# Performance work log

Measured on AMD Instinct MI355X. Metric: run time of the kernel, lower is better.

## Reference

```python
import jax, jax.numpy as jnp
import numpy as np

B, S, D, H = 4, 2048, 256, 8
DH = D // H
DFF = 4 * D
EPS = 1e-5


def _layernorm(x, w, b):
    mu = jnp.mean(x, axis=-1, keepdims=True)
    var = jnp.mean((x - mu) ** 2, axis=-1, keepdims=True)
    return (x - mu) * jax.lax.rsqrt(var + EPS) * w + b


def setup_inputs() -> dict:
    key = jax.random.key(0)
    ks = jax.random.split(key, 16)
    s = 0.02
    return {
        "x": jax.random.normal(ks[0], (B, S, D), jnp.float32),
        "in_proj_w": jax.random.normal(ks[1], (3 * D, D), jnp.float32) * s,
        "in_proj_b": jax.random.normal(ks[2], (3 * D,), jnp.float32) * s,
        "out_w": jax.random.normal(ks[3], (D, D), jnp.float32) * s,
        "out_b": jax.random.normal(ks[4], (D,), jnp.float32) * s,
        "ln1_w": jnp.ones((D,), jnp.float32),
        "ln1_b": jnp.zeros((D,), jnp.float32),
        "ln2_w": jnp.ones((D,), jnp.float32),
        "ln2_b": jnp.zeros((D,), jnp.float32),
        "ff1_w": jax.random.normal(ks[5], (DFF, D), jnp.float32) * s,
        "ff1_b": jax.random.normal(ks[6], (DFF,), jnp.float32) * s,
        "ff2_w": jax.random.normal(ks[7], (D, DFF), jnp.float32) * s,
        "ff2_b": jax.random.normal(ks[8], (D,), jnp.float32) * s,
        "slopes": jax.random.normal(ks[9], (H, 1, 1), jnp.float32),
    }


def reference(x, in_proj_w, in_proj_b, out_w, out_b, ln1_w, ln1_b, ln2_w, ln2_b,
              ff1_w, ff1_b, ff2_w, ff2_b, slopes):
    # learned ALiBi-style relative bias: (H, S, S)
    pos = jnp.arange(S, dtype=jnp.float32)
    rel = jnp.abs(pos[None, :] - pos[:, None])          # (S, S)
    bias = -jnp.abs(slopes) * rel[None, :, :]           # (H, S, S)

    xn = _layernorm(x, ln1_w, ln1_b)
    qkv = jnp.einsum('bsd,ed->bse', xn, in_proj_w) + in_proj_b
    q, k, v = jnp.split(qkv, 3, axis=-1)
    # (B, H, S, DH)
    q = q.reshape(B, S, H, DH).transpose(0, 2, 1, 3)
    k = k.reshape(B, S, H, DH).transpose(0, 2, 1, 3)
    v = v.reshape(B, S, H, DH).transpose(0, 2, 1, 3)

    scores = jnp.einsum('bhqd,bhkd->bhqk', q, k) / jnp.sqrt(jnp.float32(DH))
    scores = scores + bias[None, :, :, :]
    attn = jax.nn.softmax(scores, axis=-1)
    ctx = jnp.einsum('bhqk,bhkd->bhqd', attn, v)
    ctx = ctx.transpose(0, 2, 1, 3).reshape(B, S, D)
    attn_out = jnp.einsum('bsd,ed->bse', ctx, out_w) + out_b

    x = x + attn_out
    xn2 = _layernorm(x, ln2_w, ln2_b)
    h = jnp.einsum('bsd,fd->bsf', xn2, ff1_w) + ff1_b
    h = jax.nn.gelu(h, approximate=False)
    ff_out = jnp.einsum('bsf,df->bsd', h, ff2_w) + ff2_b
    return x + ff_out
```

## Files before the change

### kernel.cpp

```cpp
#include <hip/hip_runtime.h>
#include <hip/hip_bf16.h>
#include <math.h>

#define S_LEN 2048
#define D_MODEL 256
#define N_HEADS 8
#define HEAD_DIM 32
#define D_FF 1024
#define ROWS_TOTAL 8192

typedef __attribute__((ext_vector_type(8))) short short8;
typedef __attribute__((ext_vector_type(4))) float f32x4;

__device__ inline ushort f2bf(float f) {
    unsigned u = __builtin_bit_cast(unsigned, f);
    unsigned r = (u + 0x7fffu + ((u >> 16) & 1u)) >> 16;
    return (ushort)r;
}

__device__ inline float bf2f(ushort u) {
    return __builtin_bit_cast(float, ((unsigned)u) << 16);
}

__device__ inline unsigned cvtpk(float a, float b) {
    unsigned r;
    asm("v_cvt_pk_bf16_f32 %0, %1, %2" : "=v"(r) : "v"(a), "v"(b));
    return r;
}

__global__ __launch_bounds__(256) void prep_kernel(
    const float* __restrict__ w0, const float* __restrict__ w1,
    const float* __restrict__ w2, const float* __restrict__ w3,
    ushort* __restrict__ o0, ushort* __restrict__ o1,
    ushort* __restrict__ o2, ushort* __restrict__ o3,
    const float* __restrict__ x, const float* __restrict__ lnw,
    const float* __restrict__ lnb, ushort* __restrict__ xnb) {
    int blk = blockIdx.x;
    if (blk < 768) {
        int i = blk * 256 + threadIdx.x;
        const float* src;
        ushort* dst;
        int off;
        if (i < 49152)       { src = w0; dst = o0; off = i; }
        else if (i < 65536)  { src = w1; dst = o1; off = i - 49152; }
        else if (i < 131072) { src = w2; dst = o2; off = i - 65536; }
        else                 { src = w3; dst = o3; off = i - 131072; }
        float4 v = ((const float4*)src)[off];
        ushort4 u = {f2bf(v.x), f2bf(v.y), f2bf(v.z), f2bf(v.w)};
        ((ushort4*)dst)[off] = u;
    } else {
        int wid = threadIdx.x >> 6, lane = threadIdx.x & 63;
        int row = (blk - 768) * 4 + wid;
        float4 v = ((const float4*)(x + (size_t)row * D_MODEL))[lane];
        float4 wv = ((const float4*)lnw)[lane];
        float4 bv = ((const float4*)lnb)[lane];
        float s = v.x + v.y + v.z + v.w;
        float s2 = v.x * v.x + v.y * v.y + v.z * v.z + v.w * v.w;
        #pragma unroll
        for (int off = 1; off < 64; off <<= 1) {
            s  += __shfl_xor(s, off);
            s2 += __shfl_xor(s2, off);
        }
        float mu = s * (1.0f / D_MODEL);
        float var = s2 * (1.0f / D_MODEL) - mu * mu;
        float rstd = rsqrtf(var + 1e-5f);
        ushort4 o = {f2bf((v.x - mu) * rstd * wv.x + bv.x), f2bf((v.y - mu) * rstd * wv.y + bv.y),
                     f2bf((v.z - mu) * rstd * wv.z + bv.z), f2bf((v.w - mu) * rstd * wv.w + bv.w)};
        ((ushort4*)(xnb + (size_t)row * D_MODEL))[lane] = o;
    }
}

template <int EPI, int BM, int BN>
__global__ __launch_bounds__(256) void gemm_mfma(
    const ushort* __restrict__ A,
    const ushort* __restrict__ W,
    const float* __restrict__ bias,
    const void* __restrict__ resid,
    float* __restrict__ outf,
    ushort* __restrict__ outh,
    ushort* __restrict__ qout, ushort* __restrict__ kout, ushort* __restrict__ vout,
    int M, int N, int K) {
    constexpr int MR = BM / 32;
    constexpr int NR = BN / 32;
    __shared__ ushort As[BM * 64];
    __shared__ ushort Bs[BN * 64];
    const int tid = threadIdx.x;
    const int lane = tid & 63, wid = tid >> 6;
    const int l15 = lane & 15, hi = lane >> 4;
    const int wr = wid >> 1, wc = wid & 1;
    const int row0 = blockIdx.x * BM, col0 = blockIdx.y * BN;

    f32x4 acc[MR][NR];
    #pragma unroll
    for (int m = 0; m < MR; m++)
        #pragma unroll
        for (int n = 0; n < NR; n++) acc[m][n] = (f32x4){0.f, 0.f, 0.f, 0.f};

    short8 sa[MR], sb[NR];
    #pragma unroll
    for (int t = 0; t < MR; t++) {
        int c = tid + t * 256;
        sa[t] = *(const short8*)(A + (size_t)(row0 + (c >> 3)) * K + (c & 7) * 8);
    }
    #pragma unroll
    for (int t = 0; t < NR; t++) {
        int c = tid + t * 256;
        sb[t] = *(const short8*)(W + (size_t)(col0 + (c >> 3)) * K + (c & 7) * 8);
    }

    for (int k0 = 0; k0 < K; k0 += 64) {
        __syncthreads();
        #pragma unroll
        for (int t = 0; t < MR; t++) {
            int c = tid + t * 256;
            int r = c >> 3, cb = (c & 7) * 16;
            *(short8*)((char*)As + r * 128 + (cb ^ ((r & 7) << 4))) = sa[t];
        }
        #pragma unroll
        for (int t = 0; t < NR; t++) {
            int c = tid + t * 256;
            int r = c >> 3, cb = (c & 7) * 16;
            *(short8*)((char*)Bs + r * 128 + (cb ^ ((r & 7) << 4))) = sb[t];
        }
        __syncthreads();
        if (k0 + 64 < K) {
            #pragma unroll
            for (int t = 0; t < MR; t++) {
                int c = tid + t * 256;
                sa[t] = *(const short8*)(A + (size_t)(row0 + (c >> 3)) * K + k0 + 64 + (c & 7) * 8);
            }
            #pragma unroll
            for (int t = 0; t < NR; t++) {
                int c = tid + t * 256;
                sb[t] = *(const short8*)(W + (size_t)(col0 + (c >> 3)) * K + k0 + 64 + (c & 7) * 8);
            }
        }
        #pragma unroll
        for (int ks = 0; ks < 2; ks++) {
            short8 af[MR], bfr[NR];
            #pragma unroll
            for (int m = 0; m < MR; m++) {
                int r = wr * (BM / 2) + m * 16 + l15;
                af[m] = *(const short8*)((char*)As + r * 128 + ((ks * 64 + hi * 16) ^ ((r & 7) << 4)));
            }
            #pragma unroll
            for (int n = 0; n < NR; n++) {
                int r = wc * (BN / 2) + n * 16 + l15;
                bfr[n] = *(const short8*)((char*)Bs + r * 128 + ((ks * 64 + hi * 16) ^ ((r & 7) << 4)));
            }
            #pragma unroll
            for (int m = 0; m < MR; m++)
                #pragma unroll
                for (int n = 0; n < NR; n++)
                    acc[m][n] = __builtin_amdgcn_mfma_f32_16x16x32_bf16(af[m], bfr[n], acc[m][n], 0, 0, 0);
        }
    }

    #pragma unroll
    for (int m = 0; m < MR; m++) {
        #pragma unroll
        for (int n = 0; n < NR; n++) {
            #pragma unroll
            for (int r = 0; r < 4; r++) {
                int row = row0 + wr * (BM / 2) + m * 16 + hi * 4 + r;
                int col = col0 + wc * (BN / 2) + n * 16 + l15;
                float val = acc[m][n][r] + bias[col];
                if (EPI == 0) {
                    int part = col >> 8;
                    int d_o = col & 255;
                    int hh = d_o >> 5, dh = d_o & 31;
                    int bbb = row >> 11, s = row & 2047;
                    size_t bhi = (size_t)bbb * N_HEADS + hh;
                    if (part == 0) {
                        qout[(bhi * S_LEN + s) * HEAD_DIM + dh] = f2bf(val * 0.2550347137f);
                    } else {
                        int tt = s >> 6, k = s & 63;
                        size_t tb = (bhi * 32 + tt) * 2048;
                        if (part == 1)
                            kout[tb + (dh >> 3) * 512 + k * 8 + (dh & 7)] = f2bf(val);
                        else
                            vout[tb + ((size_t)((k >> 5) * 4 + ((k >> 3) & 3))) * 256 + dh * 8 + (k & 7)] = f2bf(val);
                    }
                } else if (EPI == 2) {
                    float g = 0.5f * val * (1.f + erff(val * 0.70710678118654752f));
                    outh[(size_t)row * N + col] = f2bf(g);
                } else {
                    float rv = bf2f(((const ushort*)resid)[(size_t)row * N + col]);
                    outf[(size_t)row * N + col] = rv + val;
                }
            }
        }
    }
}

__global__ __launch_bounds__(256) void gemm_opln(
    const ushort* __restrict__ A,
    const ushort* __restrict__ W,
    const float* __restrict__ bias,
    const float* __restrict__ residf,
    const float* __restrict__ lnw, const float* __restrict__ lnb,
    ushort* __restrict__ xnb, ushort* __restrict__ x1b) {
    __shared__ ushort As[16 * 64];
    __shared__ ushort Bs[256 * 64];
    __shared__ float red[4][16][2];
    const int tid = threadIdx.x;
    const int lane = tid & 63, wc = tid >> 6;
    const int l15 = lane & 15, hi = lane >> 4;
    const int row0 = blockIdx.x * 16;

    f32x4 acc[4];
    #pragma unroll
    for (int n = 0; n < 4; n++) acc[n] = (f32x4){0.f, 0.f, 0.f, 0.f};

    short8 sa, sb[8];
    if (tid < 128)
        sa = *(const short8*)(A + (size_t)(row0 + (tid >> 3)) * 256 + (tid & 7) * 8);
    #pragma unroll
    for (int t = 0; t < 8; t++) {
        int c = tid + t * 256;
        sb[t] = *(const short8*)(W + (size_t)(c >> 3) * 256 + (c & 7) * 8);
    }

    for (int k0 = 0; k0 < 256; k0 += 64) {
        __syncthreads();
        if (tid < 128) {
            int r = tid >> 3, cb = (tid & 7) * 16;
            *(short8*)((char*)As + r * 128 + (cb ^ ((r & 7) << 4))) = sa;
        }
        #pragma unroll
        for (int t = 0; t < 8; t++) {
            int c = tid + t * 256;
            int r = c >> 3, cb = (c & 7) * 16;
            *(short8*)((char*)Bs + r * 128 + (cb ^ ((r & 7) << 4))) = sb[t];
        }
        __syncthreads();
        if (k0 + 64 < 256) {
            if (tid < 128)
                sa = *(const short8*)(A + (size_t)(row0 + (tid >> 3)) * 256 + k0 + 64 + (tid & 7) * 8);
            #pragma unroll
            for (int t = 0; t < 8; t++) {
                int c = tid + t * 256;
                sb[t] = *(const short8*)(W + (size_t)(c >> 3) * 256 + k0 + 64 + (c & 7) * 8);
            }
        }
        #pragma unroll
        for (int ks = 0; ks < 2; ks++) {
            short8 af, bfr[4];
            {
                int r = l15;
                af = *(const short8*)((char*)As + r * 128 + ((ks * 64 + hi * 16) ^ ((r & 7) << 4)));
            }
            #pragma unroll
            for (int n = 0; n < 4; n++) {
                int r = wc * 64 + n * 16 + l15;
                bfr[n] = *(const short8*)((char*)Bs + r * 128 + ((ks * 64 + hi * 16) ^ ((r & 7) << 4)));
            }
            #pragma unroll
            for (int n = 0; n < 4; n++)
                acc[n] = __builtin_amdgcn_mfma_f32_16x16x32_bf16(af, bfr[n], acc[n], 0, 0, 0);
        }
    }

    float x1v[4][4];
    float s1[4], s2[4];
    #pragma unroll
    for (int r = 0; r < 4; r++) { s1[r] = 0.f; s2[r] = 0.f; }
    #pragma unroll
    for (int n = 0; n < 4; n++) {
        #pragma unroll
        for (int r = 0; r < 4; r++) {
            int row = row0 + hi * 4 + r;
            int col = wc * 64 + n * 16 + l15;
            float v = acc[n][r] + bias[col] + residf[(size_t)row * 256 + col];
            x1v[n][r] = v;
            s1[r] += v;
            s2[r] += v * v;
        }
    }
    #pragma unroll
    for (int r = 0; r < 4; r++) {
        #pragma unroll
        for (int off = 1; off < 16; off <<= 1) {
            s1[r] += __shfl_xor(s1[r], off);
            s2[r] += __shfl_xor(s2[r], off);
        }
    }
    if (l15 == 0) {
        #pragma unroll
        for (int r = 0; r < 4; r++) {
            red[wc][hi * 4 + r][0] = s1[r];
            red[wc][hi * 4 + r][1] = s2[r];
        }
    }
    __syncthreads();
    #pragma unroll
    for (int r = 0; r < 4; r++) {
        int rl = hi * 4 + r;
        float a1 = red[0][rl][0] + red[1][rl][0] + red[2][rl][0] + red[3][rl][0];
        float a2 = red[0][rl][1] + red[1][rl][1] + red[2][rl][1] + red[3][rl][1];
        float mu = a1 * (1.0f / 256.f);
        float var = a2 * (1.0f / 256.f) - mu * mu;
        float rstd = rsqrtf(var + 1e-5f);
        size_t row = row0 + rl;
        #pragma unroll
        for (int n = 0; n < 4; n++) {
            int col = wc * 64 + n * 16 + l15;
            float v = x1v[n][r];
            xnb[row * 256 + col] = f2bf((v - mu) * rstd * lnw[col] + lnb[col]);
            x1b[row * 256 + col] = f2bf(v);
        }
    }
}

__global__ __launch_bounds__(256) void attn_mfma(
    const ushort* __restrict__ qb, const ushort* __restrict__ kb,
    const ushort* __restrict__ vt, const float* __restrict__ slopes,
    ushort* __restrict__ ctxout) {
    __shared__ ushort plds[4][1024];
    const int tid = threadIdx.x;
    const int wid = tid >> 6, lane = tid & 63;
    const int l15 = lane & 15, hi = lane >> 4;
    const int bh = blockIdx.y, h = bh & (N_HEADS - 1), bb = bh >> 3;
    const int qt = blockIdx.x * 4 + wid;
    const int qbase = qt * 16;
    const float slope = fabsf(slopes[h]) * 1.4426950408889634f;

    const int wl = (int)fminf(2048.f, 32.f / fmaxf(slope, 1e-6f));
    const int tlo = max(0, (qbase - wl) >> 6);
    const int thi = min(31, (qbase + 15 + wl) >> 6);

    const ushort* Kg = kb + (size_t)bh * 32 * 2048;
    const ushort* Vg = vt + (size_t)bh * 32 * 2048;

    short8 qf = *(const short8*)(qb + ((size_t)bh * S_LEN + qbase + l15) * HEAD_DIM + hi * 8);

    f32x4 ctxa[2];
    ctxa[0] = (f32x4){0.f, 0.f, 0.f, 0.f};
    ctxa[1] = (f32x4){0.f, 0.f, 0.f, 0.f};
    float lsum = 0.f;

    char* pw = (char*)&plds[wid][0];
    const int bpi = lane & 0x30;
    const int wr_off = ((hi >> 1) << 8) + (l15 << 4) + ((hi & 1) << 3);
    const int rd0 = (hi << 8) + (l15 << 4);

    const float qoff = (float)(qbase + l15 - 4 * hi);

    short8 kfc[4], vfc[2][2];
    {
        const ushort* Kt = Kg + (size_t)tlo * 2048;
        const ushort* Vt = Vg + (size_t)tlo * 2048;
        #pragma unroll
        for (int c = 0; c < 4; c++)
            kfc[c] = *(const short8*)(Kt + (hi * 64 + 16 * c + l15) * 8);
        #pragma unroll
        for (int f = 0; f < 2; f++)
            #pragma unroll
            for (int dt = 0; dt < 2; dt++)
                vfc[f][dt] = *(const short8*)(Vt + ((f * 4 + hi) * 32 + dt * 16 + l15) * 8);
    }

    for (int t = tlo; t <= thi; ++t) {
// ... 46 lines not shown
        short8 pa1 = *(const short8*)(pw + 1024 + rd0);
        __builtin_amdgcn_s_setprio(1);
        #pragma unroll
        for (int dt = 0; dt < 2; dt++) {
            ctxa[dt] = __builtin_amdgcn_mfma_f32_16x16x32_bf16(pa0, vfc[0][dt], ctxa[dt], 0, 0, 0);
            ctxa[dt] = __builtin_amdgcn_mfma_f32_16x16x32_bf16(pa1, vfc[1][dt], ctxa[dt], 0, 0, 0);
        }
        __builtin_amdgcn_s_setprio(0);

        #pragma unroll
        for (int c = 0; c < 4; c++) kfc[c] = kfn[c];
        #pragma unroll
        for (int f = 0; f < 2; f++)
            #pragma unroll
            for (int dt = 0; dt < 2; dt++) vfc[f][dt] = vfn[f][dt];
    }
    float inv = 1.f / lsum;
    int invi = __builtin_bit_cast(int, inv);
    #pragma unroll
    for (int r = 0; r < 4; r++) {
        float ir = __builtin_bit_cast(float, __builtin_amdgcn_ds_bpermute(bpi + 4 * r, invi));
        size_t row = (size_t)bb * S_LEN + qbase + 4 * hi + r;
        #pragma unroll
        for (int dt = 0; dt < 2; dt++)
            ctxout[row * D_MODEL + h * HEAD_DIM + dt * 16 + l15] = f2bf(ctxa[dt][r] * ir);
    }
}

extern "C" void kernel_launch(void* const* d_in, const int* in_sizes, int n_in,
                              void* d_out, int out_size, void* d_ws, size_t ws_size,
                              hipStream_t stream) {
    const float* x      = (const float*)d_in[0];
    const float* in_w   = (const float*)d_in[1];
    const float* in_b   = (const float*)d_in[2];
    const float* outw   = (const float*)d_in[3];
    const float* outb   = (const float*)d_in[4];
    const float* ln1w   = (const float*)d_in[5];
    const float* ln1b   = (const float*)d_in[6];
    const float* ln2w   = (const float*)d_in[7];
    const float* ln2b   = (const float*)d_in[8];
    const float* ff1w   = (const float*)d_in[9];
    const float* ff1b   = (const float*)d_in[10];
    const float* ff2w   = (const float*)d_in[11];
    const float* ff2b   = (const float*)d_in[12];
    const float* slopes = (const float*)d_in[13];
    float* out = (float*)d_out;

    const size_t SZ = (size_t)ROWS_TOTAL * D_MODEL;
    ushort* xnb   = (ushort*)d_ws;
    ushort* ctxb  = xnb + SZ;
    ushort* qb16  = ctxb + SZ;
    ushort* kb16  = qb16 + SZ;
    ushort* vt16  = kb16 + SZ;
    ushort* hbb   = vt16 + SZ;
    ushort* wqkvb = hbb + 4 * SZ;
    ushort* woutb = wqkvb + 768 * 256;
    ushort* wff1b = woutb + 256 * 256;
    ushort* wff2b = wff1b + 1024 * 256;
    ushort* x1b   = wff2b + 256 * 1024;

    prep_kernel<<<768 + ROWS_TOTAL / 4, 256, 0, stream>>>(
        in_w, outw, ff1w, ff2w, wqkvb, woutb, wff1b, wff2b, x, ln1w, ln1b, xnb);
    gemm_mfma<0, 64, 128><<<dim3(ROWS_TOTAL / 64, 768 / 128), 256, 0, stream>>>(
        xnb, wqkvb, in_b, nullptr, nullptr, nullptr, qb16, kb16, vt16, ROWS_TOTAL, 768, D_MODEL);
    attn_mfma<<<dim3(32, 32), 256, 0, stream>>>(qb16, kb16, vt16, slopes, ctxb);
    gemm_opln<<<ROWS_TOTAL / 16, 256, 0, stream>>>(
        ctxb, woutb, outb, x, ln2w, ln2b, xnb, x1b);
    gemm_mfma<2, 64, 128><<<dim3(ROWS_TOTAL / 64, D_FF / 128), 256, 0, stream>>>(
        xnb, wff1b, ff1b, nullptr, nullptr, hbb, nullptr, nullptr, nullptr, ROWS_TOTAL, D_FF, D_MODEL);
    gemm_mfma<5, 64, 64><<<dim3(ROWS_TOTAL / 64, D_MODEL / 64), 256, 0, stream>>>(
        hbb, wff2b, ff2b, x1b, out, nullptr, nullptr, nullptr, nullptr, ROWS_TOTAL, D_MODEL, D_FF);
}
```

Baseline: 74.85 us.

## Fuse FFN into one kernel and prepack weights into MFMA fragment layout

```diff
diff --git a/kernel.cpp b/kernel.cpp
--- a/kernel.cpp
+++ b/kernel.cpp
@@ -26,6 +26,16 @@
     unsigned r;
     asm("v_cvt_pk_bf16_f32 %0, %1, %2" : "=v"(r) : "v"(a), "v"(b));
     return r;
+}
+
+__device__ inline void cvt_frag(const float* __restrict__ src, ushort* __restrict__ dst,
+                                int off, int kshift, int NT) {
+    float4 v = ((const float4*)src)[off];
+    int n = off >> kshift;
+    int k = (off & ((1 << kshift) - 1)) << 2;
+    int idx = (((k >> 5) * NT + (n >> 4)) << 9) + (((k >> 3) & 3) << 7) + ((n & 15) << 3) + (k & 7);
+    ushort4 u = {f2bf(v.x), f2bf(v.y), f2bf(v.z), f2bf(v.w)};
+    *(ushort4*)(dst + idx) = u;
 }
 
 __global__ __launch_bounds__(256) void prep_kernel(
@@ -38,16 +48,10 @@
     int blk = blockIdx.x;
     if (blk < 768) {
         int i = blk * 256 + threadIdx.x;
-        const float* src;
-        ushort* dst;
-        int off;
-        if (i < 49152)       { src = w0; dst = o0; off = i; }
-        else if (i < 65536)  { src = w1; dst = o1; off = i - 49152; }
-        else if (i < 131072) { src = w2; dst = o2; off = i - 65536; }
-        else                 { src = w3; dst = o3; off = i - 131072; }
-        float4 v = ((const float4*)src)[off];
-        ushort4 u = {f2bf(v.x), f2bf(v.y), f2bf(v.z), f2bf(v.w)};
-        ((ushort4*)dst)[off] = u;
+        if (i < 49152)       cvt_frag(w0, o0, i, 6, 48);
+        else if (i < 65536)  cvt_frag(w1, o1, i - 49152, 6, 16);
+        else if (i < 131072) cvt_frag(w2, o2, i - 65536, 6, 64);
+        else                 cvt_frag(w3, o3, i - 131072, 8, 16);
     } else {
         int wid = threadIdx.x >> 6, lane = threadIdx.x & 63;
         int row = (blk - 768) * 4 + wid;
@@ -70,123 +74,75 @@
     }
 }
 
-template <int EPI, int BM, int BN>
-__global__ __launch_bounds__(256) void gemm_mfma(
+__global__ __launch_bounds__(256) void gemm_qkv(
     const ushort* __restrict__ A,
-    const ushort* __restrict__ W,
+    const ushort* __restrict__ Wt,
     const float* __restrict__ bias,
-    const void* __restrict__ resid,
-    float* __restrict__ outf,
-    ushort* __restrict__ outh,
-    ushort* __restrict__ qout, ushort* __restrict__ kout, ushort* __restrict__ vout,
-    int M, int N, int K) {
-    constexpr int MR = BM / 32;
-    constexpr int NR = BN / 32;
-    __shared__ ushort As[BM * 64];
-    __shared__ ushort Bs[BN * 64];
+    ushort* __restrict__ qout, ushort* __restrict__ kout, ushort* __restrict__ vout) {
+    __shared__ ushort As[64 * 256];
     const int tid = threadIdx.x;
     const int lane = tid & 63, wid = tid >> 6;
     const int l15 = lane & 15, hi = lane >> 4;
     const int wr = wid >> 1, wc = wid & 1;
-    const int row0 = blockIdx.x * BM, col0 = blockIdx.y * BN;
-
-    f32x4 acc[MR][NR];
-    #pragma unroll
-    for (int m = 0; m < MR; m++)
-        #pragma unroll
-        for (int n = 0; n < NR; n++) acc[m][n] = (f32x4){0.f, 0.f, 0.f, 0.f};
-
-    short8 sa[MR], sb[NR];
-    #pragma unroll
-    for (int t = 0; t < MR; t++) {
+    const int row0 = blockIdx.x * 64, col0 = blockIdx.y * 128;
+
+    #pragma unroll
+    for (int t = 0; t < 8; t++) {
         int c = tid + t * 256;
-        sa[t] = *(const short8*)(A + (size_t)(row0 + (c >> 3)) * K + (c & 7) * 8);
-    }
-    #pragma unroll
-    for (int t = 0; t < NR; t++) {
-        int c = tid + t * 256;
-        sb[t] = *(const short8*)(W + (size_t)(col0 + (c >> 3)) * K + (c & 7) * 8);
-    }
-
-    for (int k0 = 0; k0 < K; k0 += 64) {
-        __syncthreads();
-        #pragma unroll
-        for (int t = 0; t < MR; t++) {
-            int c = tid + t * 256;
-            int r = c >> 3, cb = (c & 7) * 16;
-            *(short8*)((char*)As + r * 128 + (cb ^ ((r & 7) << 4))) = sa[t];
-        }
-        #pragma unroll
-        for (int t = 0; t < NR; t++) {
-            int c = tid + t * 256;
-            int r = c >> 3, cb = (c & 7) * 16;
-            *(short8*)((char*)Bs + r * 128 + (cb ^ ((r & 7) << 4))) = sb[t];
-        }
-        __syncthreads();
-        if (k0 + 64 < K) {
-            #pragma unroll
-            for (int t = 0; t < MR; t++) {
-                int c = tid + t * 256;
-                sa[t] = *(const short8*)(A + (size_t)(row0 + (c >> 3)) * K + k0 + 64 + (c & 7) * 8);
-            }
-            #pragma unroll
-            for (int t = 0; t < NR; t++) {
-                int c = tid + t * 256;
-                sb[t] = *(const short8*)(W + (size_t)(col0 + (c >> 3)) * K + k0 + 64 + (c & 7) * 8);
-            }
-        }
-        #pragma unroll
-        for (int ks = 0; ks < 2; ks++) {
-            short8 af[MR], bfr[NR];
-            #pragma unroll
-            for (int m = 0; m < MR; m++) {
-                int r = wr * (BM / 2) + m * 16 + l15;
-                af[m] = *(const short8*)((char*)As + r * 128 + ((ks * 64 + hi * 16) ^ ((r & 7) << 4)));
-            }
-            #pragma unroll
-            for (int n = 0; n < NR; n++) {
-                int r = wc * (BN / 2) + n * 16 + l15;
-                bfr[n] = *(const short8*)((char*)Bs + r * 128 + ((ks * 64 + hi * 16) ^ ((r & 7) << 4)));
-            }
-            #pragma unroll
-            for (int m = 0; m < MR; m++)
-                #pragma unroll
-                for (int n = 0; n < NR; n++)
-                    acc[m][n] = __builtin_amdgcn_mfma_f32_16x16x32_bf16(af[m], bfr[n], acc[m][n], 0, 0, 0);
-        }
-    }
-
-    #pragma unroll
-    for (int m = 0; m < MR; m++) {
-        #pragma unroll
-        for (int n = 0; n < NR; n++) {
+        int r = c >> 5, cb = (c & 31) * 16;
+        short8 va = *(const short8*)(A + (size_t)(row0 + r) * 256 + (c & 31) * 8);
+        *(short8*)((char*)As + r * 512 + (cb ^ ((r & 7) << 4))) = va;
+    }
+    __syncthreads();
+
+    f32x4 acc[2][4];
+    #pragma unroll
+    for (int m = 0; m < 2; m++)
+        #pragma unroll
+        for (int n = 0; n < 4; n++) acc[m][n] = (f32x4){0.f, 0.f, 0.f, 0.f};
+
+    const int tn0 = (col0 >> 4) + wc * 4;
+    #pragma unroll
+    for (int tk = 0; tk < 8; tk++) {
+        short8 af[2], bfr[4];
+        #pragma unroll
+        for (int m = 0; m < 2; m++) {
+            int r = wr * 32 + m * 16 + l15;
+            af[m] = *(const short8*)((char*)As + r * 512 + ((tk * 64 + hi * 16) ^ ((r & 7) << 4)));
+        }
+        #pragma unroll
+        for (int n = 0; n < 4; n++)
+            bfr[n] = *(const short8*)(Wt + (((size_t)tk * 48 + tn0 + n) << 9) + lane * 8);
+        #pragma unroll
+        for (int m = 0; m < 2; m++)
+            #pragma unroll
+            for (int n = 0; n < 4; n++)
+                acc[m][n] = __builtin_amdgcn_mfma_f32_16x16x32_bf16(af[m], bfr[n], acc[m][n], 0, 0, 0);
+    }
+
+    #pragma unroll
+    for (int m = 0; m < 2; m++) {
+        #pragma unroll
+        for (int n = 0; n < 4; n++) {
             #pragma unroll
             for (int r = 0; r < 4; r++) {
-                int row = row0 + wr * (BM / 2) + m * 16 + hi * 4 + r;
-                int col = col0 + wc * (BN / 2) + n * 16 + l15;
+                int row = row0 + wr * 32 + m * 16 + hi * 4 + r;
+                int col = col0 + wc * 64 + n * 16 + l15;
                 float val = acc[m][n][r] + bias[col];
-                if (EPI == 0) {
-                    int part = col >> 8;
-                    int d_o = col & 255;
-                    int hh = d_o >> 5, dh = d_o & 31;
-                    int bbb = row >> 11, s = row & 2047;
-                    size_t bhi = (size_t)bbb * N_HEADS + hh;
-                    if (part == 0) {
-                        qout[(bhi * S_LEN + s) * HEAD_DIM + dh] = f2bf(val * 0.2550347137f);
-                    } else {
-                        int tt = s >> 6, k = s & 63;
-                        size_t tb = (bhi * 32 + tt) * 2048;
-                        if (part == 1)
-                            kout[tb + (dh >> 3) * 512 + k * 8 + (dh & 7)] = f2bf(val);
-                        else
-                            vout[tb + ((size_t)((k >> 5) * 4 + ((k >> 3) & 3))) * 256 + dh * 8 + (k & 7)] = f2bf(val);
-                    }
-                } else if (EPI == 2) {
-                    float g = 0.5f * val * (1.f + erff(val * 0.70710678118654752f));
-                    outh[(size_t)row * N + col] = f2bf(g);
+                int part = col >> 8;
+                int d_o = col & 255;
+                int hh = d_o >> 5, dh = d_o & 31;
+                int bbb = row >> 11, s = row & 2047;
+                size_t bhi = (size_t)bbb * N_HEADS + hh;
+                if (part == 0) {
+                    qout[(bhi * S_LEN + s) * HEAD_DIM + dh] = f2bf(val * 0.2550347137f);
                 } else {
-                    float rv = bf2f(((const ushort*)resid)[(size_t)row * N + col]);
-                    outf[(size_t)row * N + col] = rv + val;
+                    int tt = s >> 6, k = s & 63;
+                    size_t tb = (bhi * 32 + tt) * 2048;
+                    if (part == 1)
+                        kout[tb + (dh >> 3) * 512 + k * 8 + (dh & 7)] = f2bf(val);
+                    else
+                        vout[tb + ((size_t)((k >> 5) * 4 + ((k >> 3) & 3))) * 256 + dh * 8 + (k & 7)] = f2bf(val);
                 }
             }
         }
@@ -195,69 +151,38 @@
 
 __global__ __launch_bounds__(256) void gemm_opln(
     const ushort* __restrict__ A,
-    const ushort* __restrict__ W,
+    const ushort* __restrict__ Wt,
     const float* __restrict__ bias,
     const float* __restrict__ residf,
     const float* __restrict__ lnw, const float* __restrict__ lnb,
     ushort* __restrict__ xnb, ushort* __restrict__ x1b) {
-    __shared__ ushort As[16 * 64];
-    __shared__ ushort Bs[256 * 64];
+    __shared__ ushort As[16 * 256];
     __shared__ float red[4][16][2];
     const int tid = threadIdx.x;
-    const int lane = tid & 63, wc = tid >> 6;
+    const int lane = tid & 63, wid = tid >> 6;
     const int l15 = lane & 15, hi = lane >> 4;
     const int row0 = blockIdx.x * 16;
 
+    #pragma unroll
+    for (int t = 0; t < 2; t++) {
+        int c = tid + t * 256;
+        int r = c >> 5, cb = (c & 31) * 16;
+        short8 va = *(const short8*)(A + (size_t)(row0 + r) * 256 + (c & 31) * 8);
+        *(short8*)((char*)As + r * 512 + (cb ^ ((r & 7) << 4))) = va;
+    }
+    __syncthreads();
+
     f32x4 acc[4];
     #pragma unroll
     for (int n = 0; n < 4; n++) acc[n] = (f32x4){0.f, 0.f, 0.f, 0.f};
 
-    short8 sa, sb[8];
-    if (tid < 128)
-        sa = *(const short8*)(A + (size_t)(row0 + (tid >> 3)) * 256 + (tid & 7) * 8);
-    #pragma unroll
-    for (int t = 0; t < 8; t++) {
-        int c = tid + t * 256;
-        sb[t] = *(const short8*)(W + (size_t)(c >> 3) * 256 + (c & 7) * 8);
-    }
-
-    for (int k0 = 0; k0 < 256; k0 += 64) {
-        __syncthreads();
-        if (tid < 128) {
-            int r = tid >> 3, cb = (tid & 7) * 16;
-            *(short8*)((char*)As + r * 128 + (cb ^ ((r & 7) << 4))) = sa;
-        }
-        #pragma unroll
-        for (int t = 0; t < 8; t++) {
-            int c = tid + t * 256;
-            int r = c >> 3, cb = (c & 7) * 16;
-            *(short8*)((char*)Bs + r * 128 + (cb ^ ((r & 7) << 4))) = sb[t];
-        }
-        __syncthreads();
-        if (k0 + 64 < 256) {
-            if (tid < 128)
-                sa = *(const short8*)(A + (size_t)(row0 + (tid >> 3)) * 256 + k0 + 64 + (tid & 7) * 8);
-            #pragma unroll
-            for (int t = 0; t < 8; t++) {
-                int c = tid + t * 256;
-                sb[t] = *(const short8*)(W + (size_t)(c >> 3) * 256 + k0 + 64 + (c & 7) * 8);
-            }
-        }
-        #pragma unroll
-        for (int ks = 0; ks < 2; ks++) {
-            short8 af, bfr[4];
-            {
-                int r = l15;
-                af = *(const short8*)((char*)As + r * 128 + ((ks * 64 + hi * 16) ^ ((r & 7) << 4)));
-            }
-            #pragma unroll
-            for (int n = 0; n < 4; n++) {
-                int r = wc * 64 + n * 16 + l15;
-                bfr[n] = *(const short8*)((char*)Bs + r * 128 + ((ks * 64 + hi * 16) ^ ((r & 7) << 4)));
-            }
-            #pragma unroll
-            for (int n = 0; n < 4; n++)
-                acc[n] = __builtin_amdgcn_mfma_f32_16x16x32_bf16(af, bfr[n], acc[n], 0, 0, 0);
+    #pragma unroll
+    for (int tk = 0; tk < 8; tk++) {
+        short8 af = *(const short8*)((char*)As + l15 * 512 + ((tk * 64 + hi * 16) ^ ((l15 & 7) << 4)));
+        #pragma unroll
+        for (int n = 0; n < 4; n++) {
+            short8 bfr = *(const short8*)(Wt + (((size_t)tk * 16 + wid * 4 + n) << 9) + lane * 8);
+            acc[n] = __builtin_amdgcn_mfma_f32_16x16x32_bf16(af, bfr, acc[n], 0, 0, 0);
         }
     }
 
@@ -270,7 +195,7 @@
         #pragma unroll
         for (int r = 0; r < 4; r++) {
             int row = row0 + hi * 4 + r;
-            int col = wc * 64 + n * 16 + l15;
+            int col = wid * 64 + n * 16 + l15;
             float v = acc[n][r] + bias[col] + residf[(size_t)row * 256 + col];
             x1v[n][r] = v;
             s1[r] += v;
@@ -288,8 +213,8 @@
     if (l15 == 0) {
         #pragma unroll
         for (int r = 0; r < 4; r++) {
-            red[wc][hi * 4 + r][0] = s1[r];
-            red[wc][hi * 4 + r][1] = s2[r];
+            red[wid][hi * 4 + r][0] = s1[r];
+            red[wid][hi * 4 + r][1] = s2[r];
         }
     }
     __syncthreads();
@@ -304,10 +229,93 @@
         size_t row = row0 + rl;
         #pragma unroll
         for (int n = 0; n < 4; n++) {
-            int col = wc * 64 + n * 16 + l15;
+            int col = wid * 64 + n * 16 + l15;
             float v = x1v[n][r];
             xnb[row * 256 + col] = f2bf((v - mu) * rstd * lnw[col] + lnb[col]);
             x1b[row * 256 + col] = f2bf(v);
+        }
+    }
+}
+
+__global__ __launch_bounds__(256) void ffn_kernel(
+    const ushort* __restrict__ A,
+    const ushort* __restrict__ W1t,
+    const ushort* __restrict__ W2t,
+    const float* __restrict__ b1, const float* __restrict__ b2,
+    const ushort* __restrict__ x1b,
+    float* __restrict__ out) {
+    __shared__ ushort As[16 * 256];
+    __shared__ ushort Hs[2048];
+    const int tid = threadIdx.x;
+    const int lane = tid & 63, wid = tid >> 6;
+    const int l15 = lane & 15, hi = lane >> 4;
+    const int row0 = blockIdx.x * 16;
+
+    #pragma unroll
+    for (int t = 0; t < 2; t++) {
+        int c = tid + t * 256;
+        int r = c >> 5, cb = (c & 31) * 16;
+        short8 va = *(const short8*)(A + (size_t)(row0 + r) * 256 + (c & 31) * 8);
+        *(short8*)((char*)As + r * 512 + (cb ^ ((r & 7) << 4))) = va;
+    }
+    __syncthreads();
+
+    f32x4 acc[4];
+    #pragma unroll
+    for (int n = 0; n < 4; n++) acc[n] = (f32x4){0.f, 0.f, 0.f, 0.f};
+
+    const int hwr = (4 * wid + (hi >> 1)) * 256 + l15 * 16 + (hi & 1) * 8;
+
+    for (int ch = 0; ch < 8; ch++) {
+        f32x4 hacc[2];
+        hacc[0] = (f32x4){0.f, 0.f, 0.f, 0.f};
+        hacc[1] = (f32x4){0.f, 0.f, 0.f, 0.f};
+        #pragma unroll
+        for (int tk = 0; tk < 8; tk++) {
+            short8 xb = *(const short8*)((char*)As + l15 * 512 + ((tk * 64 + hi * 16) ^ ((l15 & 7) << 4)));
+            #pragma unroll
+            for (int nf = 0; nf < 2; nf++) {
+                int tnf = ch * 8 + wid * 2 + nf;
+                short8 fa = *(const short8*)(W1t + (((size_t)tk * 64 + tnf) << 9) + lane * 8);
+                hacc[nf] = __builtin_amdgcn_mfma_f32_16x16x32_bf16(fa, xb, hacc[nf], 0, 0, 0);
+            }
+        }
+        __syncthreads();
+        #pragma unroll
+        for (int nf = 0; nf < 2; nf++) {
+            int fcb = ch * 128 + wid * 32 + nf * 16 + hi * 4;
+            float g[4];
+            #pragma unroll
+            for (int r = 0; r < 4; r++) {
+                float v = hacc[nf][r] + b1[fcb + r];
+                g[r] = 0.5f * v * (1.f + erff(v * 0.70710678118654752f));
+            }
+            unsigned lo  = cvtpk(g[0], g[1]);
+            unsigned hi2 = cvtpk(g[2], g[3]);
+            *(unsigned long long*)((char*)Hs + (nf << 9) + hwr) =
+                ((unsigned long long)hi2 << 32) | (unsigned long long)lo;
+        }
+        __syncthreads();
+        #pragma unroll
+        for (int s = 0; s < 4; s++) {
+            short8 pa = *(const short8*)((char*)Hs + (4 * s + hi) * 256 + l15 * 16);
+            int tk2 = ch * 4 + s;
+            #pragma unroll
+            for (int n = 0; n < 4; n++) {
+                short8 bfr = *(const short8*)(W2t + (((size_t)tk2 * 16 + wid * 4 + n) << 9) + lane * 8);
+                acc[n] = __builtin_amdgcn_mfma_f32_16x16x32_bf16(pa, bfr, acc[n], 0, 0, 0);
+            }
+        }
+    }
+
+    #pragma unroll
+    for (int n = 0; n < 4; n++) {
+        #pragma unroll
+        for (int r = 0; r < 4; r++) {
+            size_t row = row0 + hi * 4 + r;
+            int col = wid * 64 + n * 16 + l15;
+            float rv = bf2f(x1b[row * 256 + col]);
+            out[row * 256 + col] = acc[n][r] + b2[col] + rv;
         }
     }
 }
@@ -460,22 +468,19 @@
     ushort* qb16  = ctxb + SZ;
     ushort* kb16  = qb16 + SZ;
     ushort* vt16  = kb16 + SZ;
-    ushort* hbb   = vt16 + SZ;
-    ushort* wqkvb = hbb + 4 * SZ;
-    ushort* woutb = wqkvb + 768 * 256;
-    ushort* wff1b = woutb + 256 * 256;
-    ushort* wff2b = wff1b + 1024 * 256;
-    ushort* x1b   = wff2b + 256 * 1024;
+    ushort* x1b   = vt16 + SZ;
+    ushort* wqkvt = x1b + SZ;
+    ushort* woutt = wqkvt + 768 * 256;
+    ushort* wff1t = woutt + 256 * 256;
+    ushort* wff2t = wff1t + 1024 * 256;
 
     prep_kernel<<<768 + ROWS_TOTAL / 4, 256, 0, stream>>>(
-        in_w, outw, ff1w, ff2w, wqkvb, woutb, wff1b, wff2b, x, ln1w, ln1b, xnb);
-    gemm_mfma<0, 64, 128><<<dim3(ROWS_TOTAL / 64, 768 / 128), 256, 0, stream>>>(
-        xnb, wqkvb, in_b, nullptr, nullptr, nullptr, qb16, kb16, vt16, ROWS_TOTAL, 768, D_MODEL);
+        in_w, outw, ff1w, ff2w, wqkvt, woutt, wff1t, wff2t, x, ln1w, ln1b, xnb);
+    gemm_qkv<<<dim3(ROWS_TOTAL / 64, 6), 256, 0, stream>>>(
+        xnb, wqkvt, in_b, qb16, kb16, vt16);
     attn_mfma<<<dim3(32, 32), 256, 0, stream>>>(qb16, kb16, vt16, slopes, ctxb);
     gemm_opln<<<ROWS_TOTAL / 16, 256, 0, stream>>>(
-        ctxb, woutb, outb, x, ln2w, ln2b, xnb, x1b);
-    gemm_mfma<2, 64, 128><<<dim3(ROWS_TOTAL / 64, D_FF / 128), 256, 0, stream>>>(
-        xnb, wff1b, ff1b, nullptr, nullptr, hbb, nullptr, nullptr, nullptr, ROWS_TOTAL, D_FF, D_MODEL);
-    gemm_mfma<5, 64, 64><<<dim3(ROWS_TOTAL / 64, D_MODEL / 64), 256, 0, stream>>>(
-        hbb, wff2b, ff2b, x1b, out, nullptr, nullptr, nullptr, nullptr, ROWS_TOTAL, D_MODEL, D_FF);
-}
+        ctxb, woutt, outb, x, ln2w, ln2b, xnb, x1b);
+    ffn_kernel<<<ROWS_TOTAL / 16, 256, 0, stream>>>(
+        xnb, wff1t, wff2t, ff1b, ff2b, x1b, out);
+}
```

Measured after the change: 84.65 us. +13.1%, slower.

## Drop prep kernel: fuse LN1 into QKV GEMM and convert fp32 weights on load

Applied to the files above, without the earlier changes.

```diff
diff --git a/kernel.cpp b/kernel.cpp
--- a/kernel.cpp
+++ b/kernel.cpp
@@ -28,165 +28,129 @@
     return r;
 }
 
-__global__ __launch_bounds__(256) void prep_kernel(
-    const float* __restrict__ w0, const float* __restrict__ w1,
-    const float* __restrict__ w2, const float* __restrict__ w3,
-    ushort* __restrict__ o0, ushort* __restrict__ o1,
-    ushort* __restrict__ o2, ushort* __restrict__ o3,
+__device__ inline short8 cvt8(float4 a, float4 b) {
+    union { unsigned u[4]; short8 s; } r;
+    r.u[0] = cvtpk(a.x, a.y);
+    r.u[1] = cvtpk(a.z, a.w);
+    r.u[2] = cvtpk(b.x, b.y);
+    r.u[3] = cvtpk(b.z, b.w);
+    return r.s;
+}
+
+__global__ __launch_bounds__(256) void qkv_ln(
     const float* __restrict__ x, const float* __restrict__ lnw,
-    const float* __restrict__ lnb, ushort* __restrict__ xnb) {
-    int blk = blockIdx.x;
-    if (blk < 768) {
-        int i = blk * 256 + threadIdx.x;
-        const float* src;
-        ushort* dst;
-        int off;
-        if (i < 49152)       { src = w0; dst = o0; off = i; }
-        else if (i < 65536)  { src = w1; dst = o1; off = i - 49152; }
-        else if (i < 131072) { src = w2; dst = o2; off = i - 65536; }
-        else                 { src = w3; dst = o3; off = i - 131072; }
-        float4 v = ((const float4*)src)[off];
-        ushort4 u = {f2bf(v.x), f2bf(v.y), f2bf(v.z), f2bf(v.w)};
-        ((ushort4*)dst)[off] = u;
-    } else {
-        int wid = threadIdx.x >> 6, lane = threadIdx.x & 63;
-        int row = (blk - 768) * 4 + wid;
-        float4 v = ((const float4*)(x + (size_t)row * D_MODEL))[lane];
-        float4 wv = ((const float4*)lnw)[lane];
-        float4 bv = ((const float4*)lnb)[lane];
-        float s = v.x + v.y + v.z + v.w;
-        float s2 = v.x * v.x + v.y * v.y + v.z * v.z + v.w * v.w;
-        #pragma unroll
-        for (int off = 1; off < 64; off <<= 1) {
-            s  += __shfl_xor(s, off);
-            s2 += __shfl_xor(s2, off);
-        }
-        float mu = s * (1.0f / D_MODEL);
-        float var = s2 * (1.0f / D_MODEL) - mu * mu;
-        float rstd = rsqrtf(var + 1e-5f);
-        ushort4 o = {f2bf((v.x - mu) * rstd * wv.x + bv.x), f2bf((v.y - mu) * rstd * wv.y + bv.y),
-                     f2bf((v.z - mu) * rstd * wv.z + bv.z), f2bf((v.w - mu) * rstd * wv.w + bv.w)};
-        ((ushort4*)(xnb + (size_t)row * D_MODEL))[lane] = o;
-    }
-}
-
-template <int EPI, int BM, int BN>
-__global__ __launch_bounds__(256) void gemm_mfma(
-    const ushort* __restrict__ A,
-    const ushort* __restrict__ W,
+    const float* __restrict__ lnb, const float* __restrict__ W,
     const float* __restrict__ bias,
-    const void* __restrict__ resid,
-    float* __restrict__ outf,
-    ushort* __restrict__ outh,
-    ushort* __restrict__ qout, ushort* __restrict__ kout, ushort* __restrict__ vout,
-    int M, int N, int K) {
-    constexpr int MR = BM / 32;
-    constexpr int NR = BN / 32;
-    __shared__ ushort As[BM * 64];
-    __shared__ ushort Bs[BN * 64];
+    ushort* __restrict__ qout, ushort* __restrict__ kout, ushort* __restrict__ vout) {
+    __shared__ ushort As[64 * 256];
+    __shared__ ushort Bs[128 * 64];
     const int tid = threadIdx.x;
     const int lane = tid & 63, wid = tid >> 6;
     const int l15 = lane & 15, hi = lane >> 4;
     const int wr = wid >> 1, wc = wid & 1;
-    const int row0 = blockIdx.x * BM, col0 = blockIdx.y * BN;
-
-    f32x4 acc[MR][NR];
-    #pragma unroll
-    for (int m = 0; m < MR; m++)
-        #pragma unroll
-        for (int n = 0; n < NR; n++) acc[m][n] = (f32x4){0.f, 0.f, 0.f, 0.f};
-
-    short8 sa[MR], sb[NR];
-    #pragma unroll
-    for (int t = 0; t < MR; t++) {
+    const int row0 = blockIdx.x * 64, col0 = blockIdx.y * 128;
+
+    float4 wv = ((const float4*)lnw)[lane];
+    float4 bv = ((const float4*)lnb)[lane];
+    const int cb = lane * 8;
+    for (int rr = 0; rr < 16; rr++) {
+        int r = (wid << 4) + rr;
+        float4 v = ((const float4*)(x + (size_t)(row0 + r) * 256))[lane];
+        float s = v.x + v.y + v.z + v.w;
+        float s2 = v.x * v.x + v.y * v.y + v.z * v.z + v.w * v.w;
+        #pragma unroll
+        for (int off = 1; off < 64; off <<= 1) {
+            s  += __shfl_xor(s, off);
+            s2 += __shfl_xor(s2, off);
+        }
+        float mu = s * (1.0f / 256.f);
+        float rstd = rsqrtf(s2 * (1.0f / 256.f) - mu * mu + 1e-5f);
+        unsigned lo  = cvtpk((v.x - mu) * rstd * wv.x + bv.x, (v.y - mu) * rstd * wv.y + bv.y);
+        unsigned hi2 = cvtpk((v.z - mu) * rstd * wv.z + bv.z, (v.w - mu) * rstd * wv.w + bv.w);
+        int sw = (((cb & ~15) ^ ((r & 7) << 4)) | (cb & 8));
+        *(unsigned long long*)((char*)As + r * 512 + sw) =
+            ((unsigned long long)hi2 << 32) | (unsigned long long)lo;
+    }
+
+    f32x4 acc[2][4];
+    #pragma unroll
+    for (int m = 0; m < 2; m++)
+        #pragma unroll
+        for (int n = 0; n < 4; n++) acc[m][n] = (f32x4){0.f, 0.f, 0.f, 0.f};
+
+    float4 pb[4][2];
+    #pragma unroll
+    for (int t = 0; t < 4; t++) {
         int c = tid + t * 256;
-        sa[t] = *(const short8*)(A + (size_t)(row0 + (c >> 3)) * K + (c & 7) * 8);
-    }
-    #pragma unroll
-    for (int t = 0; t < NR; t++) {
-        int c = tid + t * 256;
-        sb[t] = *(const short8*)(W + (size_t)(col0 + (c >> 3)) * K + (c & 7) * 8);
-    }
-
-    for (int k0 = 0; k0 < K; k0 += 64) {
-        __syncthreads();
-        #pragma unroll
-        for (int t = 0; t < MR; t++) {
+        const float* src = W + (size_t)(col0 + (c >> 3)) * 256 + (c & 7) * 8;
+        pb[t][0] = *(const float4*)src;
+        pb[t][1] = *(const float4*)(src + 4);
+    }
+    __syncthreads();
+
+    for (int ch = 0; ch < 4; ch++) {
+        #pragma unroll
+        for (int t = 0; t < 4; t++) {
             int c = tid + t * 256;
-            int r = c >> 3, cb = (c & 7) * 16;
-            *(short8*)((char*)As + r * 128 + (cb ^ ((r & 7) << 4))) = sa[t];
-        }
-        #pragma unroll
-        for (int t = 0; t < NR; t++) {
-            int c = tid + t * 256;
-            int r = c >> 3, cb = (c & 7) * 16;
-            *(short8*)((char*)Bs + r * 128 + (cb ^ ((r & 7) << 4))) = sb[t];
-        }
-        __syncthreads();
-        if (k0 + 64 < K) {
-            #pragma unroll
-            for (int t = 0; t < MR; t++) {
+            int r = c >> 3, cbb = (c & 7) * 16;
+            *(short8*)((char*)Bs + r * 128 + (cbb ^ ((r & 7) << 4))) = cvt8(pb[t][0], pb[t][1]);
+        }
+        __syncthreads();
+        if (ch < 3) {
+            #pragma unroll
+            for (int t = 0; t < 4; t++) {
                 int c = tid + t * 256;
-                sa[t] = *(const short8*)(A + (size_t)(row0 + (c >> 3)) * K + k0 + 64 + (c & 7) * 8);
-            }
-            #pragma unroll
-            for (int t = 0; t < NR; t++) {
-                int c = tid + t * 256;
-                sb[t] = *(const short8*)(W + (size_t)(col0 + (c >> 3)) * K + k0 + 64 + (c & 7) * 8);
+                const float* src = W + (size_t)(col0 + (c >> 3)) * 256 + (ch + 1) * 64 + (c & 7) * 8;
+                pb[t][0] = *(const float4*)src;
+                pb[t][1] = *(const float4*)(src + 4);
             }
         }
         #pragma unroll
         for (int ks = 0; ks < 2; ks++) {
-            short8 af[MR], bfr[NR];
-            #pragma unroll
-            for (int m = 0; m < MR; m++) {
-                int r = wr * (BM / 2) + m * 16 + l15;
-                af[m] = *(const short8*)((char*)As + r * 128 + ((ks * 64 + hi * 16) ^ ((r & 7) << 4)));
-            }
-            #pragma unroll
-            for (int n = 0; n < NR; n++) {
-                int r = wc * (BN / 2) + n * 16 + l15;
+            int tk = ch * 2 + ks;
+            short8 af[2], bfr[4];
+            #pragma unroll
+            for (int m = 0; m < 2; m++) {
+                int r = wr * 32 + m * 16 + l15;
+                af[m] = *(const short8*)((char*)As + r * 512 + ((tk * 64 + hi * 16) ^ ((r & 7) << 4)));
+            }
+            #pragma unroll
+            for (int n = 0; n < 4; n++) {
+                int r = wc * 64 + n * 16 + l15;
                 bfr[n] = *(const short8*)((char*)Bs + r * 128 + ((ks * 64 + hi * 16) ^ ((r & 7) << 4)));
             }
             #pragma unroll
-            for (int m = 0; m < MR; m++)
+            for (int m = 0; m < 2; m++)
                 #pragma unroll
-                for (int n = 0; n < NR; n++)
+                for (int n = 0; n < 4; n++)
                     acc[m][n] = __builtin_amdgcn_mfma_f32_16x16x32_bf16(af[m], bfr[n], acc[m][n], 0, 0, 0);
         }
-    }
-
-    #pragma unroll
-    for (int m = 0; m < MR; m++) {
-        #pragma unroll
-        for (int n = 0; n < NR; n++) {
+        __syncthreads();
+    }
+
+    #pragma unroll
+    for (int m = 0; m < 2; m++) {
+        #pragma unroll
+        for (int n = 0; n < 4; n++) {
             #pragma unroll
             for (int r = 0; r < 4; r++) {
-                int row = row0 + wr * (BM / 2) + m * 16 + hi * 4 + r;
-                int col = col0 + wc * (BN / 2) + n * 16 + l15;
+                int row = row0 + wr * 32 + m * 16 + hi * 4 + r;
+                int col = col0 + wc * 64 + n * 16 + l15;
                 float val = acc[m][n][r] + bias[col];
-                if (EPI == 0) {
-                    int part = col >> 8;
-                    int d_o = col & 255;
-                    int hh = d_o >> 5, dh = d_o & 31;
-                    int bbb = row >> 11, s = row & 2047;
-                    size_t bhi = (size_t)bbb * N_HEADS + hh;
-                    if (part == 0) {
-                        qout[(bhi * S_LEN + s) * HEAD_DIM + dh] = f2bf(val * 0.2550347137f);
-                    } else {
-                        int tt = s >> 6, k = s & 63;
-                        size_t tb = (bhi * 32 + tt) * 2048;
-                        if (part == 1)
-                            kout[tb + (dh >> 3) * 512 + k * 8 + (dh & 7)] = f2bf(val);
-                        else
-                            vout[tb + ((size_t)((k >> 5) * 4 + ((k >> 3) & 3))) * 256 + dh * 8 + (k & 7)] = f2bf(val);
-                    }
-                } else if (EPI == 2) {
-                    float g = 0.5f * val * (1.f + erff(val * 0.70710678118654752f));
-                    outh[(size_t)row * N + col] = f2bf(g);
+                int part = col >> 8;
+                int d_o = col & 255;
+                int hh = d_o >> 5, dh = d_o & 31;
+                int bbb = row >> 11, s = row & 2047;
+                size_t bhi = (size_t)bbb * N_HEADS + hh;
+                if (part == 0) {
+                    qout[(bhi * S_LEN + s) * HEAD_DIM + dh] = f2bf(val * 0.2550347137f);
                 } else {
-                    float rv = bf2f(((const ushort*)resid)[(size_t)row * N + col]);
-                    outf[(size_t)row * N + col] = rv + val;
+                    int tt = s >> 6, k = s & 63;
+                    size_t tb = (bhi * 32 + tt) * 2048;
+                    if (part == 1)
+                        kout[tb + (dh >> 3) * 512 + k * 8 + (dh & 7)] = f2bf(val);
+                    else
+                        vout[tb + ((size_t)((k >> 5) * 4 + ((k >> 3) & 3))) * 256 + dh * 8 + (k & 7)] = f2bf(val);
                 }
             }
         }
@@ -195,7 +159,7 @@
 
 __global__ __launch_bounds__(256) void gemm_opln(
     const ushort* __restrict__ A,
-    const ushort* __restrict__ W,
+    const float* __restrict__ W,
     const float* __restrict__ bias,
     const float* __restrict__ residf,
     const float* __restrict__ lnw, const float* __restrict__ lnb,
@@ -212,13 +176,16 @@
     #pragma unroll
     for (int n = 0; n < 4; n++) acc[n] = (f32x4){0.f, 0.f, 0.f, 0.f};
 
-    short8 sa, sb[8];
+    short8 sa;
+    float4 pb[8][2];
     if (tid < 128)
         sa = *(const short8*)(A + (size_t)(row0 + (tid >> 3)) * 256 + (tid & 7) * 8);
     #pragma unroll
     for (int t = 0; t < 8; t++) {
         int c = tid + t * 256;
-        sb[t] = *(const short8*)(W + (size_t)(c >> 3) * 256 + (c & 7) * 8);
+        const float* src = W + (size_t)(c >> 3) * 256 + (c & 7) * 8;
+        pb[t][0] = *(const float4*)src;
+        pb[t][1] = *(const float4*)(src + 4);
     }
 
     for (int k0 = 0; k0 < 256; k0 += 64) {
@@ -231,7 +198,7 @@
         for (int t = 0; t < 8; t++) {
             int c = tid + t * 256;
             int r = c >> 3, cb = (c & 7) * 16;
-            *(short8*)((char*)Bs + r * 128 + (cb ^ ((r & 7) << 4))) = sb[t];
+            *(short8*)((char*)Bs + r * 128 + (cb ^ ((r & 7) << 4))) = cvt8(pb[t][0], pb[t][1]);
         }
         __syncthreads();
         if (k0 + 64 < 256) {
@@ -240,7 +207,9 @@
             #pragma unroll
             for (int t = 0; t < 8; t++) {
                 int c = tid + t * 256;
-                sb[t] = *(const short8*)(W + (size_t)(c >> 3) * 256 + k0 + 64 + (c & 7) * 8);
+                const float* src = W + (size_t)(c >> 3) * 256 + k0 + 64 + (c & 7) * 8;
+                pb[t][0] = *(const float4*)src;
+                pb[t][1] = *(const float4*)(src + 4);
             }
         }
         #pragma unroll
@@ -308,6 +277,186 @@
             float v = x1v[n][r];
             xnb[row * 256 + col] = f2bf((v - mu) * rstd * lnw[col] + lnb[col]);
             x1b[row * 256 + col] = f2bf(v);
+        }
+    }
+}
+
+__global__ __launch_bounds__(256) void gemm_ff1(
+    const ushort* __restrict__ A,
+    const float* __restrict__ W,
+    const float* __restrict__ bias,
+    ushort* __restrict__ outh) {
+    __shared__ ushort As[64 * 256];
+    __shared__ ushort Bs[128 * 64];
+    const int tid = threadIdx.x;
+    const int lane = tid & 63, wid = tid >> 6;
+    const int l15 = lane & 15, hi = lane >> 4;
+    const int wr = wid >> 1, wc = wid & 1;
+    const int row0 = blockIdx.x * 64, col0 = blockIdx.y * 128;
+
+    #pragma unroll
+    for (int t = 0; t < 8; t++) {
+        int c = tid + t * 256;
+        int r = c >> 5, cb = (c & 31) * 16;
+        short8 va = *(const short8*)(A + (size_t)(row0 + r) * 256 + (c & 31) * 8);
+        *(short8*)((char*)As + r * 512 + (cb ^ ((r & 7) << 4))) = va;
+    }
+
+    f32x4 acc[2][4];
+    #pragma unroll
+    for (int m = 0; m < 2; m++)
+        #pragma unroll
+        for (int n = 0; n < 4; n++) acc[m][n] = (f32x4){0.f, 0.f, 0.f, 0.f};
+
+    float4 pb[4][2];
+    #pragma unroll
+    for (int t = 0; t < 4; t++) {
+        int c = tid + t * 256;
+        const float* src = W + (size_t)(col0 + (c >> 3)) * 256 + (c & 7) * 8;
+        pb[t][0] = *(const float4*)src;
+        pb[t][1] = *(const float4*)(src + 4);
+    }
+    __syncthreads();
+
+    for (int ch = 0; ch < 4; ch++) {
+        #pragma unroll
+        for (int t = 0; t < 4; t++) {
+            int c = tid + t * 256;
+            int r = c >> 3, cbb = (c & 7) * 16;
+            *(short8*)((char*)Bs + r * 128 + (cbb ^ ((r & 7) << 4))) = cvt8(pb[t][0], pb[t][1]);
+        }
+        __syncthreads();
+        if (ch < 3) {
+            #pragma unroll
+            for (int t = 0; t < 4; t++) {
+                int c = tid + t * 256;
+                const float* src = W + (size_t)(col0 + (c >> 3)) * 256 + (ch + 1) * 64 + (c & 7) * 8;
+                pb[t][0] = *(const float4*)src;
+                pb[t][1] = *(const float4*)(src + 4);
+            }
+        }
+        #pragma unroll
+        for (int ks = 0; ks < 2; ks++) {
+            int tk = ch * 2 + ks;
+            short8 af[2], bfr[4];
+            #pragma unroll
+            for (int m = 0; m < 2; m++) {
+                int r = wr * 32 + m * 16 + l15;
+                af[m] = *(const short8*)((char*)As + r * 512 + ((tk * 64 + hi * 16) ^ ((r & 7) << 4)));
+            }
+            #pragma unroll
+            for (int n = 0; n < 4; n++) {
+                int r = wc * 64 + n * 16 + l15;
+                bfr[n] = *(const short8*)((char*)Bs + r * 128 + ((ks * 64 + hi * 16) ^ ((r & 7) << 4)));
+            }
+            #pragma unroll
+            for (int m = 0; m < 2; m++)
+                #pragma unroll
+                for (int n = 0; n < 4; n++)
+                    acc[m][n] = __builtin_amdgcn_mfma_f32_16x16x32_bf16(af[m], bfr[n], acc[m][n], 0, 0, 0);
+        }
+        __syncthreads();
+    }
+
+    #pragma unroll
+    for (int m = 0; m < 2; m++) {
+        #pragma unroll
+        for (int n = 0; n < 4; n++) {
+            #pragma unroll
+            for (int r = 0; r < 4; r++) {
+                int row = row0 + wr * 32 + m * 16 + hi * 4 + r;
+                int col = col0 + wc * 64 + n * 16 + l15;
+                float val = acc[m][n][r] + bias[col];
+                float g = 0.5f * val * (1.f + erff(val * 0.70710678118654752f));
+                outh[(size_t)row * D_FF + col] = f2bf(g);
+            }
+        }
+    }
+}
+
+__global__ __launch_bounds__(256) void gemm_ff2(
+    const ushort* __restrict__ A,
+    const float* __restrict__ W,
+    const float* __restrict__ bias,
+    const ushort* __restrict__ resid,
+    float* __restrict__ outf) {
+    __shared__ ushort As[64 * 64];
+    __shared__ ushort Bs[64 * 64];
+    const int tid = threadIdx.x;
+    const int lane = tid & 63, wid = tid >> 6;
+    const int l15 = lane & 15, hi = lane >> 4;
+    const int wr = wid >> 1, wc = wid & 1;
+    const int row0 = blockIdx.x * 64, col0 = blockIdx.y * 64;
+
+    f32x4 acc[2][2];
+    #pragma unroll
+    for (int m = 0; m < 2; m++)
+        #pragma unroll
+        for (int n = 0; n < 2; n++) acc[m][n] = (f32x4){0.f, 0.f, 0.f, 0.f};
+
+    short8 sa[2];
+    float4 pb[2][2];
+    #pragma unroll
+    for (int t = 0; t < 2; t++) {
+        int c = tid + t * 256;
+        sa[t] = *(const short8*)(A + (size_t)(row0 + (c >> 3)) * 1024 + (c & 7) * 8);
+        const float* src = W + (size_t)(col0 + (c >> 3)) * 1024 + (c & 7) * 8;
+        pb[t][0] = *(const float4*)src;
+        pb[t][1] = *(const float4*)(src + 4);
+    }
+
+    for (int k0 = 0; k0 < 1024; k0 += 64) {
+        __syncthreads();
+        #pragma unroll
+        for (int t = 0; t < 2; t++) {
+            int c = tid + t * 256;
+            int r = c >> 3, cb = (c & 7) * 16;
+            *(short8*)((char*)As + r * 128 + (cb ^ ((r & 7) << 4))) = sa[t];
+            *(short8*)((char*)Bs + r * 128 + (cb ^ ((r & 7) << 4))) = cvt8(pb[t][0], pb[t][1]);
+        }
+        __syncthreads();
+        if (k0 + 64 < 1024) {
+            #pragma unroll
+            for (int t = 0; t < 2; t++) {
+                int c = tid + t * 256;
+                sa[t] = *(const short8*)(A + (size_t)(row0 + (c >> 3)) * 1024 + k0 + 64 + (c & 7) * 8);
+                const float* src = W + (size_t)(col0 + (c >> 3)) * 1024 + k0 + 64 + (c & 7) * 8;
+                pb[t][0] = *(const float4*)src;
+                pb[t][1] = *(const float4*)(src + 4);
+            }
+        }
+        #pragma unroll
+        for (int ks = 0; ks < 2; ks++) {
+            short8 af[2], bfr[2];
+            #pragma unroll
+            for (int m = 0; m < 2; m++) {
+                int r = wr * 32 + m * 16 + l15;
+                af[m] = *(const short8*)((char*)As + r * 128 + ((ks * 64 + hi * 16) ^ ((r & 7) << 4)));
+            }
+            #pragma unroll
+            for (int n = 0; n < 2; n++) {
+                int r = wc * 32 + n * 16 + l15;
+                bfr[n] = *(const short8*)((char*)Bs + r * 128 + ((ks * 64 + hi * 16) ^ ((r & 7) << 4)));
+            }
+            #pragma unroll
+            for (int m = 0; m < 2; m++)
+                #pragma unroll
+                for (int n = 0; n < 2; n++)
+                    acc[m][n] = __builtin_amdgcn_mfma_f32_16x16x32_bf16(af[m], bfr[n], acc[m][n], 0, 0, 0);
+        }
+    }
+
+    #pragma unroll
+    for (int m = 0; m < 2; m++) {
+        #pragma unroll
+        for (int n = 0; n < 2; n++) {
+            #pragma unroll
+            for (int r = 0; r < 4; r++) {
+                int row = row0 + wr * 32 + m * 16 + hi * 4 + r;
+                int col = col0 + wc * 32 + n * 16 + l15;
+                float rv = bf2f(resid[(size_t)row * 256 + col]);
+                outf[(size_t)row * 256 + col] = acc[m][n][r] + bias[col] + rv;
+            }
         }
     }
 }
@@ -460,22 +609,16 @@
     ushort* qb16  = ctxb + SZ;
     ushort* kb16  = qb16 + SZ;
     ushort* vt16  = kb16 + SZ;
-    ushort* hbb   = vt16 + SZ;
-    ushort* wqkvb = hbb + 4 * SZ;
-    ushort* woutb = wqkvb + 768 * 256;
-    ushort* wff1b = woutb + 256 * 256;
-    ushort* wff2b = wff1b + 1024 * 256;
-    ushort* x1b   = wff2b + 256 * 1024;
-
-    prep_kernel<<<768 + ROWS_TOTAL / 4, 256, 0, stream>>>(
-        in_w, outw, ff1w, ff2w, wqkvb, woutb, wff1b, wff2b, x, ln1w, ln1b, xnb);
-    gemm_mfma<0, 64, 128><<<dim3(ROWS_TOTAL / 64, 768 / 128), 256, 0, stream>>>(
-        xnb, wqkvb, in_b, nullptr, nullptr, nullptr, qb16, kb16, vt16, ROWS_TOTAL, 768, D_MODEL);
+    ushort* x1b   = vt16 + SZ;
+    ushort* hbb   = x1b + SZ;
+
+    qkv_ln<<<dim3(ROWS_TOTAL / 64, 6), 256, 0, stream>>>(
+        x, ln1w, ln1b, in_w, in_b, qb16, kb16, vt16);
     attn_mfma<<<dim3(32, 32), 256, 0, stream>>>(qb16, kb16, vt16, slopes, ctxb);
     gemm_opln<<<ROWS_TOTAL / 16, 256, 0, stream>>>(
-        ctxb, woutb, outb, x, ln2w, ln2b, xnb, x1b);
-    gemm_mfma<2, 64, 128><<<dim3(ROWS_TOTAL / 64, D_FF / 128), 256, 0, stream>>>(
-        xnb, wff1b, ff1b, nullptr, nullptr, hbb, nullptr, nullptr, nullptr, ROWS_TOTAL, D_FF, D_MODEL);
-    gemm_mfma<5, 64, 64><<<dim3(ROWS_TOTAL / 64, D_MODEL / 64), 256, 0, stream>>>(
-        hbb, wff2b, ff2b, x1b, out, nullptr, nullptr, nullptr, nullptr, ROWS_TOTAL, D_MODEL, D_FF);
-}
+        ctxb, outw, outb, x, ln2w, ln2b, xnb, x1b);
+    gemm_ff1<<<dim3(ROWS_TOTAL / 64, D_FF / 128), 256, 0, stream>>>(
+        xnb, ff1w, ff1b, hbb);
+    gemm_ff2<<<dim3(ROWS_TOTAL / 64, D_MODEL / 64), 256, 0, stream>>>(
+        hbb, ff2w, ff2b, x1b, out);
+}
```

Result: slower. 86.48 us (+15.5%).
